# Optimization experiments

Measured on AMD Instinct MI355X. Metric: run time of the kernel, lower is better.

## Reference

```python
import jax, jax.numpy as jnp
import numpy as np

N = 100000
IN_DIM = 64
OUT_DIM = 64
NUM_TYPES = 64


def setup_inputs() -> dict:
    key = jax.random.key(0)
    kx, kt, km, kb = jax.random.split(key, 4)
    x = jax.random.normal(kx, (N, IN_DIM), dtype=jnp.float32)
    types = jax.random.randint(kt, (N,), 0, NUM_TYPES, dtype=jnp.int64)
    # kaiming_uniform with a=sqrt(5) -> bound = sqrt(6/((1+5)*fan_in)) = 1/sqrt(fan_in)
    w_bound = 1.0 / np.sqrt(IN_DIM)
    matrix = jax.random.uniform(km, (NUM_TYPES, IN_DIM, OUT_DIM), dtype=jnp.float32,
                                minval=-w_bound, maxval=w_bound)
    b_bound = 1.0 / np.sqrt(IN_DIM)
    bias = jax.random.uniform(kb, (NUM_TYPES, OUT_DIM), dtype=jnp.float32,
                              minval=-b_bound, maxval=b_bound)
    return {"x": x, "types": types, "matrix": matrix, "bias": bias}


def reference(x, types, matrix, bias):
    # Gather per-atom weight matrices: (N, in, out), then batched matvec.
    out = jnp.einsum('ni,nio->no', x, matrix[types])  # (N, out)
    out = out + bias[types]                            # per-type bias
    return out
```

## Files before the change

### kernel.cpp

```cpp
#include <hip/hip_runtime.h>
#include <hip/hip_bf16.h>

#define NTYPES 64
#define DIM 64
#define HB 64
#define MT_STR 72

typedef short bf16x8 __attribute__((ext_vector_type(8)));
typedef float f32x4  __attribute__((ext_vector_type(4)));

static __device__ __forceinline__ short f2bf(float f) {
    __hip_bfloat16 h = __float2bfloat16(f);
    return *reinterpret_cast<short*>(&h);
}

__global__ void hist_k(const int* __restrict__ types, int n, int* __restrict__ part) {
    __shared__ int lh[NTYPES];
    int tid = threadIdx.x;
    if (tid < NTYPES) lh[tid] = 0;
    __syncthreads();
    for (int i = blockIdx.x * blockDim.x + tid; i < n; i += gridDim.x * blockDim.x)
        atomicAdd(&lh[types[i]], 1);
    __syncthreads();
    if (tid < NTYPES) part[blockIdx.x * NTYPES + tid] = lh[tid];
}

__global__ void scan_k(const int* __restrict__ part, int* __restrict__ start,
                       int* __restrict__ cursor) {
    __shared__ int ps[4][NTYPES];
    int tid = threadIdx.x;
    int t = tid & 63, seg = tid >> 6;
    int s = 0;
    #pragma unroll
    for (int i = 0; i < HB / 4; ++i)
        s += part[(seg * (HB / 4) + i) * NTYPES + t];
    ps[seg][t] = s;
    __syncthreads();
    if (tid < 64) {
        int sum = ps[0][t] + ps[1][t] + ps[2][t] + ps[3][t];
        int inc = sum;
        #pragma unroll
        for (int d = 1; d < 64; d <<= 1) {
            int u = __shfl_up(inc, d);
            if (t >= d) inc += u;
        }
        int exc = inc - sum;
        start[t] = exc;
        cursor[t] = exc;
        if (t == 63) start[NTYPES] = inc;
    }
}

__global__ void scatter_k(const int* __restrict__ types, int n, int* __restrict__ cursor,
                          int* __restrict__ perm) {
    __shared__ int lh[NTYPES];
    __shared__ int lbase[NTYPES];
    int tid = threadIdx.x;
    if (tid < NTYPES) lh[tid] = 0;
    __syncthreads();
    const int PER = 4;
    int base = blockIdx.x * blockDim.x * PER;
    int myt[PER], myo[PER];
    #pragma unroll
    for (int k = 0; k < PER; ++k) {
        int i = base + k * blockDim.x + tid;
        if (i < n) {
            int t = types[i];
            myt[k] = t;
            myo[k] = atomicAdd(&lh[t], 1);
        } else {
            myt[k] = -1;
        }
    }
    __syncthreads();
    if (tid < NTYPES) lbase[tid] = lh[tid] ? atomicAdd(&cursor[tid], lh[tid]) : 0;
    __syncthreads();
    #pragma unroll
    for (int k = 0; k < PER; ++k)
        if (myt[k] >= 0)
            perm[lbase[myt[k]] + myo[k]] = base + k * blockDim.x + tid;
}

__global__ __launch_bounds__(256) void main_k(const float* __restrict__ x,
                                              const float* __restrict__ M,
                                              const float* __restrict__ bias,
                                              const int* __restrict__ start,
                                              const int* __restrict__ perm,
                                              float* __restrict__ out) {
    int t = blockIdx.x;
    int s0 = start[t];
    int cnt = start[t + 1] - s0;
    if ((int)blockIdx.y * 64 >= cnt) return;

    int tid = threadIdx.x;
    int lane = tid & 63;
    int wave = tid >> 6;
    int col  = lane & 15;
    int hi   = lane >> 4;

    __shared__ __align__(16) short Mt[DIM * MT_STR];

    {
        const float4* Msrc = (const float4*)(M + ((size_t)t << 12));
        #pragma unroll
        for (int i = 0; i < 4; ++i) {
            int f  = tid + 256 * i;
            int k  = f >> 4;
            int o4 = (f & 15) * 4;
            float4 v = Msrc[f];
            Mt[(o4 + 0) * MT_STR + k] = f2bf(v.x);
            Mt[(o4 + 1) * MT_STR + k] = f2bf(v.y);
            Mt[(o4 + 2) * MT_STR + k] = f2bf(v.z);
            Mt[(o4 + 3) * MT_STR + k] = f2bf(v.w);
        }
    }

    float bcol[4];
    #pragma unroll
    for (int ct = 0; ct < 4; ++ct) bcol[ct] = bias[t * DIM + ct * 16 + col];

    __syncthreads();

    int lim = s0 + cnt;
    for (int bb = blockIdx.y; bb * 64 < cnt; bb += gridDim.y) {
        int abase = s0 + bb * 64;
        int nA = cnt - bb * 64; if (nA > 64) nA = 64;

        int aidx = abase + wave * 16 + col;
        if (aidx >= lim) aidx = s0;
        int g = perm[aidx];
        const float* xr = x + ((size_t)g << 6);
        float4 p0 = *(const float4*)(xr + hi * 8);
        float4 p1 = *(const float4*)(xr + hi * 8 + 4);
        float4 p2 = *(const float4*)(xr + 32 + hi * 8);
        float4 p3 = *(const float4*)(xr + 32 + hi * 8 + 4);
        bf16x8 af0, af1;
        af0[0] = f2bf(p0.x); af0[1] = f2bf(p0.y); af0[2] = f2bf(p0.z); af0[3] = f2bf(p0.w);
        af0[4] = f2bf(p1.x); af0[5] = f2bf(p1.y); af0[6] = f2bf(p1.z); af0[7] = f2bf(p1.w);
        af1[0] = f2bf(p2.x); af1[1] = f2bf(p2.y); af1[2] = f2bf(p2.z); af1[3] = f2bf(p2.w);
        af1[4] = f2bf(p3.x); af1[5] = f2bf(p3.y); af1[6] = f2bf(p3.z); af1[7] = f2bf(p3.w);

        f32x4 acc[4];
        #pragma unroll
        for (int ct = 0; ct < 4; ++ct) {
            acc[ct][0] = bcol[ct]; acc[ct][1] = bcol[ct];
            acc[ct][2] = bcol[ct]; acc[ct][3] = bcol[ct];
        }
        #pragma unroll
        for (int ct = 0; ct < 4; ++ct) {
            const short* mrow = Mt + (ct * 16 + col) * MT_STR;
            bf16x8 b0 = *(const bf16x8*)(mrow + hi * 8);
            bf16x8 b1 = *(const bf16x8*)(mrow + 32 + hi * 8);
            acc[ct] = __builtin_amdgcn_mfma_f32_16x16x32_bf16(af0, b0, acc[ct], 0, 0, 0);
            acc[ct] = __builtin_amdgcn_mfma_f32_16x16x32_bf16(af1, b1, acc[ct], 0, 0, 0);
        }

        #pragma unroll
        for (int r = 0; r < 4; ++r) {
            int arow = wave * 16 + hi * 4 + r;
            if (arow < nA) {
                int g2 = perm[abase + arow];
                float* orow = out + ((size_t)g2 << 6) + col;
                #pragma unroll
                for (int ct = 0; ct < 4; ++ct)
                    orow[ct * 16] = acc[ct][r];
            }
        }
    }
}

extern "C" void kernel_launch(void* const* d_in, const int* in_sizes, int n_in,
                              void* d_out, int out_size, void* d_ws, size_t ws_size,
                              hipStream_t stream) {
    const float* x     = (const float*)d_in[0];
    const int*   types = (const int*)d_in[1];
    const float* M     = (const float*)d_in[2];
    const float* bias  = (const float*)d_in[3];
    float* out = (float*)d_out;
    int n = in_sizes[1];

    int* part   = (int*)d_ws;
    int* start  = part + HB * NTYPES;
    int* cursor = start + 65;
    int* perm   = part + HB * NTYPES + 256;

    hist_k<<<HB, 256, 0, stream>>>(types, n, part);
    scan_k<<<1, 256, 0, stream>>>(part, start, cursor);
    scatter_k<<<(n + 1023) / 1024, 256, 0, stream>>>(types, n, cursor, perm);
    main_k<<<dim3(NTYPES, 26), 256, 0, stream>>>(x, M, bias, start, perm, out);
}
```

Baseline: 95.30 us.

## Pretranspose weights to bf16 in histogram kernel and swap MFMA operand roles

Weight matrices are converted to bf16 and transposed into a global workspace inside the histogram kernel, so the main kernel no longer builds a shared-memory copy or synchronises. The main kernel now puts the weights in the A operand and the atoms in B, so each lane holds one atom's output row. It writes contiguous float4 stores and loads the bias as a vector. Work is split per wave in 16-atom tiles instead of per block in 64-atom tiles. The cost is that weight fragments are now read from global memory or L2 on every tile rather than from LDS.

New measurement: 99.26 us. 1.04x slower.

```diff
diff --git a/kernel.cpp b/kernel.cpp
--- a/kernel.cpp
+++ b/kernel.cpp
@@ -4,7 +4,6 @@
 #define NTYPES 64
 #define DIM 64
 #define HB 64
-#define MT_STR 72
 
 typedef short bf16x8 __attribute__((ext_vector_type(8)));
 typedef float f32x4  __attribute__((ext_vector_type(4)));
@@ -14,15 +13,31 @@
     return *reinterpret_cast<short*>(&h);
 }
 
-__global__ void hist_k(const int* __restrict__ types, int n, int* __restrict__ part) {
+__global__ void hist_mtr_k(const int* __restrict__ types, int n, int* __restrict__ part,
+                           const float* __restrict__ M, short* __restrict__ Mt) {
     __shared__ int lh[NTYPES];
     int tid = threadIdx.x;
+    int t = blockIdx.x;
     if (tid < NTYPES) lh[tid] = 0;
     __syncthreads();
-    for (int i = blockIdx.x * blockDim.x + tid; i < n; i += gridDim.x * blockDim.x)
+    for (int i = t * blockDim.x + tid; i < n; i += gridDim.x * blockDim.x)
         atomicAdd(&lh[types[i]], 1);
+
+    {
+        int o  = tid >> 2;
+        int ks = tid & 3;
+        const float* Ms = M + ((size_t)t << 12);
+        short vals[16];
+        #pragma unroll
+        for (int j = 0; j < 16; ++j)
+            vals[j] = f2bf(Ms[(ks * 16 + j) * DIM + o]);
+        short* dst = Mt + ((size_t)t << 12) + o * DIM + ks * 16;
+        *(bf16x8*)(dst)     = *(const bf16x8*)(vals);
+        *(bf16x8*)(dst + 8) = *(const bf16x8*)(vals + 8);
+    }
+
     __syncthreads();
-    if (tid < NTYPES) part[blockIdx.x * NTYPES + tid] = lh[tid];
+    if (tid < NTYPES) part[t * NTYPES + tid] = lh[tid];
 }
 
 __global__ void scan_k(const int* __restrict__ part, int* __restrict__ start,
@@ -82,7 +97,7 @@
 }
 
 __global__ __launch_bounds__(256) void main_k(const float* __restrict__ x,
-                                              const float* __restrict__ M,
+                                              const short* __restrict__ Mt,
                                               const float* __restrict__ bias,
                                               const int* __restrict__ start,
                                               const int* __restrict__ perm,
@@ -90,81 +105,52 @@
     int t = blockIdx.x;
     int s0 = start[t];
     int cnt = start[t + 1] - s0;
-    if ((int)blockIdx.y * 64 >= cnt) return;
+    if (cnt <= 0) return;
 
-    int tid = threadIdx.x;
+    int tid  = threadIdx.x;
     int lane = tid & 63;
     int wave = tid >> 6;
     int col  = lane & 15;
     int hi   = lane >> 4;
 
-    __shared__ __align__(16) short Mt[DIM * MT_STR];
+    const short* At = Mt + ((size_t)t << 12);
+    int nt  = (cnt + 15) >> 4;
+    int lim = s0 + cnt;
 
-    {
-        const float4* Msrc = (const float4*)(M + ((size_t)t << 12));
-        #pragma unroll
-        for (int i = 0; i < 4; ++i) {
-            int f  = tid + 256 * i;
-            int k  = f >> 4;
-            int o4 = (f & 15) * 4;
-            float4 v = Msrc[f];
-            Mt[(o4 + 0) * MT_STR + k] = f2bf(v.x);
-            Mt[(o4 + 1) * MT_STR + k] = f2bf(v.y);
-            Mt[(o4 + 2) * MT_STR + k] = f2bf(v.z);
-            Mt[(o4 + 3) * MT_STR + k] = f2bf(v.w);
-        }
-    }
+    for (int tau = blockIdx.y * 4 + wave; tau < nt; tau += gridDim.y * 4) {
+        int abase = s0 + (tau << 4);
+        int aidx  = abase + col;
+        bool valid = aidx < lim;
+        if (!valid) aidx = lim - 1;
+        int g = perm[aidx];
 
-    float bcol[4];
-    #pragma unroll
-    for (int ct = 0; ct < 4; ++ct) bcol[ct] = bias[t * DIM + ct * 16 + col];
-
-    __syncthreads();
-
-    int lim = s0 + cnt;
-    for (int bb = blockIdx.y; bb * 64 < cnt; bb += gridDim.y) {
-        int abase = s0 + bb * 64;
-        int nA = cnt - bb * 64; if (nA > 64) nA = 64;
-
-        int aidx = abase + wave * 16 + col;
-        if (aidx >= lim) aidx = s0;
-        int g = perm[aidx];
         const float* xr = x + ((size_t)g << 6);
         float4 p0 = *(const float4*)(xr + hi * 8);
         float4 p1 = *(const float4*)(xr + hi * 8 + 4);
         float4 p2 = *(const float4*)(xr + 32 + hi * 8);
         float4 p3 = *(const float4*)(xr + 32 + hi * 8 + 4);
-        bf16x8 af0, af1;
-        af0[0] = f2bf(p0.x); af0[1] = f2bf(p0.y); af0[2] = f2bf(p0.z); af0[3] = f2bf(p0.w);
-        af0[4] = f2bf(p1.x); af0[5] = f2bf(p1.y); af0[6] = f2bf(p1.z); af0[7] = f2bf(p1.w);
-        af1[0] = f2bf(p2.x); af1[1] = f2bf(p2.y); af1[2] = f2bf(p2.z); af1[3] = f2bf(p2.w);
-        af1[4] = f2bf(p3.x); af1[5] = f2bf(p3.y); af1[6] = f2bf(p3.z); af1[7] = f2bf(p3.w);
+        bf16x8 b0, b1;
+        b0[0] = f2bf(p0.x); b0[1] = f2bf(p0.y); b0[2] = f2bf(p0.z); b0[3] = f2bf(p0.w);
+        b0[4] = f2bf(p1.x); b0[5] = f2bf(p1.y); b0[6] = f2bf(p1.z); b0[7] = f2bf(p1.w);
+        b1[0] = f2bf(p2.x); b1[1] = f2bf(p2.y); b1[2] = f2bf(p2.z); b1[3] = f2bf(p2.w);
+        b1[4] = f2bf(p3.x); b1[5] = f2bf(p3.y); b1[6] = f2bf(p3.z); b1[7] = f2bf(p3.w);
 
         f32x4 acc[4];
         #pragma unroll
         for (int ct = 0; ct < 4; ++ct) {
-            acc[ct][0] = bcol[ct]; acc[ct][1] = bcol[ct];
-            acc[ct][2] = bcol[ct]; acc[ct][3] = bcol[ct];
-        }
-        #pragma unroll
-        for (int ct = 0; ct < 4; ++ct) {
-            const short* mrow = Mt + (ct * 16 + col) * MT_STR;
-            bf16x8 b0 = *(const bf16x8*)(mrow + hi * 8);
-            bf16x8 b1 = *(const bf16x8*)(mrow + 32 + hi * 8);
-            acc[ct] = __builtin_amdgcn_mfma_f32_16x16x32_bf16(af0, b0, acc[ct], 0, 0, 0);
-            acc[ct] = __builtin_amdgcn_mfma_f32_16x16x32_bf16(af1, b1, acc[ct], 0, 0, 0);
+            const short* ar = At + (ct * 16 + col) * DIM + hi * 8;
+            bf16x8 a0 = *(const bf16x8*)(ar);
+            bf16x8 a1 = *(const bf16x8*)(ar + 32);
+            acc[ct] = *(const f32x4*)(bias + t * DIM + ct * 16 + hi * 4);
+            acc[ct] = __builtin_amdgcn_mfma_f32_16x16x32_bf16(a0, b0, acc[ct], 0, 0, 0);
+            acc[ct] = __builtin_amdgcn_mfma_f32_16x16x32_bf16(a1, b1, acc[ct], 0, 0, 0);
         }
 
-        #pragma unroll
-        for (int r = 0; r < 4; ++r) {
-            int arow = wave * 16 + hi * 4 + r;
-            if (arow < nA) {
-                int g2 = perm[abase + arow];
-                float* orow = out + ((size_t)g2 << 6) + col;
-                #pragma unroll
-                for (int ct = 0; ct < 4; ++ct)
-                    orow[ct * 16] = acc[ct][r];
-            }
+        if (valid) {
+            float* orow = out + ((size_t)g << 6);
+            #pragma unroll
+            for (int ct = 0; ct < 4; ++ct)
+                *(f32x4*)(orow + ct * 16 + hi * 4) = acc[ct];
         }
     }
 }
@@ -183,9 +169,10 @@
     int* start  = part + HB * NTYPES;
     int* cursor = start + 65;
     int* perm   = part + HB * NTYPES + 256;
+    short* Mt   = (short*)(perm + ((n + 3) & ~3));
 
-    hist_k<<<HB, 256, 0, stream>>>(types, n, part);
+    hist_mtr_k<<<HB, 256, 0, stream>>>(types, n, part, M, Mt);
     scan_k<<<1, 256, 0, stream>>>(part, start, cursor);
     scatter_k<<<(n + 1023) / 1024, 256, 0, stream>>>(types, n, cursor, perm);
-    main_k<<<dim3(NTYPES, 26), 256, 0, stream>>>(x, M, bias, start, perm, out);
+    main_k<<<dim3(NTYPES, 26), 256, 0, stream>>>(x, Mt, bias, start, perm, out);
 }
```
